# Kernel tuning notes

Measured on AMD Instinct MI355X. Metric: run time of the kernel, lower is better.

## Reference

```python
import jax, jax.numpy as jnp
import numpy as np

EPS = 1e-6
NUM_HEADS = 8
FOCUS = 3.0


def setup_inputs() -> dict:
    key = jax.random.key(0)
    ks = jax.random.split(key, 8)
    B, N, C = 16, 4096, 256
    head_dim, ksz = C // NUM_HEADS, 5
    s = 1.0 / np.sqrt(C)
    return {
        "x": jax.random.normal(ks[0], (B, N, C), jnp.float32),
        "Wq": jax.random.normal(ks[1], (C, C), jnp.float32) * s,
        "Wkv": jax.random.normal(ks[2], (C, 2 * C), jnp.float32) * s,
        "Wp": jax.random.normal(ks[3], (C, C), jnp.float32) * s,
        "bp": jnp.zeros((C,), jnp.float32),
        "scale_param": jnp.zeros((1, 1, C), jnp.float32),
        "pos_enc": jax.random.normal(ks[4], (1, N, C), jnp.float32) * 0.02,
        "dwc_w": jax.random.normal(ks[5], (head_dim, 1, ksz, ksz), jnp.float32) * 0.1,
        "dwc_b": jnp.zeros((head_dim,), jnp.float32),
        "H": 64,
        "W": 64,
    }


def _focus(t, scale, f):
    # relu feature map + power focusing with norm restoration
    t = (jax.nn.relu(t) + EPS) / scale
    tn = jnp.linalg.norm(t, axis=-1, keepdims=True)
    tf = t ** f
    return tf / jnp.linalg.norm(tf, axis=-1, keepdims=True) * tn


def reference(x, Wq, Wkv, Wp, bp, scale_param, pos_enc, dwc_w, dwc_b, H, W):
    B, N, C = x.shape
    h = NUM_HEADS
    d = C // h
    n = N  # sr_ratio == 1

    q = x @ Wq                                  # [B,N,C]
    kv = x @ Wkv                                # [B,N,2C]
    k, v = kv[..., :C], kv[..., C:]
    k = k + pos_enc

    scale = jax.nn.softplus(scale_param)
    q = _focus(q, scale, FOCUS)
    k = _focus(k, scale, FOCUS)

    # split heads: [B,h,N,d]
    qh = q.reshape(B, N, h, d).transpose(0, 2, 1, 3)
    kh = k.reshape(B, n, h, d).transpose(0, 2, 1, 3)
    vh = v.reshape(B, n, h, d).transpose(0, 2, 1, 3)

    # linear attention: z = 1/(q . mean_n(k)), kv = k^T v / n, out = (q @ kv) * z
    z = 1.0 / (jnp.einsum("bhnd,bhd->bhn", qh, kh.mean(axis=2)) + EPS)
    kvmat = jnp.einsum("bhnd,bhne->bhde", kh, vh) / n     # [B,h,d,d]
    out = jnp.einsum("bhnd,bhde->bhne", qh, kvmat) * z[..., None]

    out = out.transpose(0, 2, 1, 3).reshape(B, N, C)      # [B,N,C]

    # depthwise conv on v over the HxW grid, per head-channel
    v4 = vh.reshape(B * h, H, W, d).transpose(0, 3, 1, 2)  # [B*h,d,H,W]
    conv = jax.lax.conv_general_dilated(
        v4, dwc_w, window_strides=(1, 1), padding="SAME",
        feature_group_count=d,
        dimension_numbers=("NCHW", "OIHW", "NCHW"))
    conv = conv + dwc_b[None, :, None, None]
    out = out + conv.reshape(B, C, N).transpose(0, 2, 1)

    return out @ Wp + bp
```

## Files before the change

kernel.cpp:

```cpp
#include <hip/hip_runtime.h>
#include <hip/hip_bf16.h>

typedef unsigned short u16;
using bf16_t = __hip_bfloat16;
typedef short short8 __attribute__((ext_vector_type(8)));
typedef float f32x4 __attribute__((ext_vector_type(4)));

__device__ __forceinline__ float b2f(u16 u) {
    return __uint_as_float((unsigned int)u << 16);
}
__device__ __forceinline__ u16 f2b(float f) {
    bf16_t h = __float2bfloat16(f);
    union { bf16_t h; u16 u; } cv; cv.h = h; return cv.u;
}
__device__ __forceinline__ float ldv(const void* p, size_t i, int f32) {
    return f32 ? ((const float*)p)[i] : b2f(((const u16*)p)[i]);
}
__device__ __forceinline__ uint4 pack8(float4 a, float4 b) {
    uint4 u;
    u.x = (unsigned)f2b(a.x) | ((unsigned)f2b(a.y) << 16);
    u.y = (unsigned)f2b(a.z) | ((unsigned)f2b(a.w) << 16);
    u.z = (unsigned)f2b(b.x) | ((unsigned)f2b(b.y) << 16);
    u.w = (unsigned)f2b(b.z) | ((unsigned)f2b(b.w) << 16);
    return u;
}
__device__ __forceinline__ int swz(int n, int k) {
    return k ^ ((n & 7) << 3);
}
__device__ __forceinline__ void gl16(const u16* g, u16* l) {
    __builtin_amdgcn_global_load_lds(
        (const __attribute__((address_space(1))) unsigned int*)g,
        (__attribute__((address_space(3))) unsigned int*)l, 16, 0, 0);
}

__global__ void detect_kernel(const void* __restrict__ x, int* __restrict__ flag)
{
    const int t = threadIdx.x;
    const u16 h = ((const u16*)x)[2 * t];
    const int e = (h >> 7) & 0xFF;
    const int plaus = (e >= 112 && e <= 133) ? 1 : 0;
    const unsigned long long m = __ballot(plaus);
    if (t == 0) flag[0] = (__popcll(m) < 32) ? 1 : 0;
}

__global__ __launch_bounds__(256)
void xcvt_kernel(const void* __restrict__ x, u16* __restrict__ xb,
                 const int* __restrict__ flagp)
{
    const size_t i = ((size_t)blockIdx.x * 256 + threadIdx.x) * 8;
    if (*flagp) {
        const float* xf = (const float*)x + i;
        const float4 f0 = *reinterpret_cast<const float4*>(xf);
        const float4 f1 = *reinterpret_cast<const float4*>(xf + 4);
        *reinterpret_cast<uint4*>(xb + i) = pack8(f0, f1);
    } else {
        *reinterpret_cast<uint4*>(xb + i) =
            *reinterpret_cast<const uint4*>((const u16*)x + i);
    }
}

__global__ __launch_bounds__(256)
void prep_kernel(const void* __restrict__ pe, u16* __restrict__ peb,
                 const void* __restrict__ Wq, u16* __restrict__ WqT,
                 const void* __restrict__ Wkv, u16* __restrict__ WkvT,
                 const void* __restrict__ Wp, u16* __restrict__ WpT,
                 const int* __restrict__ flagp)
{
    const int f32 = *flagp;
    __shared__ float tile[32][33];
    const int bid = blockIdx.x;
    if (bid < 1024) {
        const size_t i = ((size_t)bid * 256 + threadIdx.x) * 4;
        if (f32) {
            const float4 f = *reinterpret_cast<const float4*>((const float*)pe + i);
            ushort4 o; o.x = f2b(f.x); o.y = f2b(f.y); o.z = f2b(f.z); o.w = f2b(f.w);
            *reinterpret_cast<ushort4*>(peb + i) = o;
        } else {
            *reinterpret_cast<ushort4*>(peb + i) =
                *reinterpret_cast<const ushort4*>((const u16*)pe + i);
        }
        return;
    }
    int lb = bid - 1024;
    const void* W; u16* WT; int N;
    if (lb < 64)       { W = Wq;  WT = WqT;  N = 256; }
    else if (lb < 192) { W = Wkv; WT = WkvT; N = 512; lb -= 64; }
    else               { W = Wp;  WT = WpT;  N = 256; lb -= 192; }
    const int tx = threadIdx.x & 31, ty = threadIdx.x >> 5;
    const int bx = lb % (N >> 5);
    const int by = lb / (N >> 5);
    #pragma unroll
    for (int r = 0; r < 4; ++r) {
        const int k = by * 32 + ty + r * 8;
        const int n = bx * 32 + tx;
        tile[ty + r * 8][tx] = ldv(W, (size_t)k * N + n, f32);
    }
    __syncthreads();
    #pragma unroll
    for (int r = 0; r < 4; ++r) {
        const int n2 = bx * 32 + ty + r * 8;
        const int k2 = by * 32 + tx;
        WT[(size_t)n2 * 256 + k2] = f2b(tile[tx][ty + r * 8]);
    }
}

template<int MODE>
__global__ __launch_bounds__(256, 2)
void gemm256(const void* __restrict__ Aany, const u16* __restrict__ Abf,
             const u16* __restrict__ BT, u16* __restrict__ O0,
             const void* __restrict__ extra, const int* __restrict__ flagp,
             int abf)
{
    const int f32 = *flagp;
    __shared__ u16 As[128 * 64];
    __shared__ u16 Bs[256 * 64];
    __shared__ float red2[2][128];
    __shared__ float red6[2][128];
    __shared__ float ratio_s[128];
    __shared__ float sscr[256];

    const int tid  = threadIdx.x;
    const int row0 = blockIdx.x * 128;
    const int lane = tid & 63;
    const int wv   = tid >> 6;
    const int wvu  = __builtin_amdgcn_readfirstlane(wv);
    const int wm   = (wv & 1) * 64;
    const int wn   = (wv >> 1) * 128;
    const int l15  = lane & 15;
    const int lq   = lane >> 4;
    const int lr8  = lane >> 3;
    const int lc8  = (lane & 7) * 8;

    if (MODE == 3) {
        const float p = ldv(extra, tid, f32);
        const float s = (p > 20.f) ? p : log1pf(expf(p));
        sscr[tid] = 1.0f / s;
    }

    f32x4 acc[4][8] = {};

    for (int k0 = 0; k0 < 256; k0 += 64) {
        #pragma unroll
        for (int it = 0; it < 8; ++it) {
            const int r = wvu * 64 + it * 8 + lr8;
            gl16(BT + (size_t)r * 256 + k0 + swz(r, lc8),
                 &Bs[(wvu * 64 + it * 8) * 64]);
        }
        if (MODE == 2 || abf || !f32) {
            const u16* Ab = (MODE == 2) ? Abf : (const u16*)Aany;
            #pragma unroll
            for (int it = 0; it < 4; ++it) {
                const int r = wvu * 32 + it * 8 + lr8;
                gl16(Ab + (size_t)(row0 + r) * 256 + k0 + swz(r, lc8),
                     &As[(wvu * 32 + it * 8) * 64]);
            }
        } else {
            const int sr = tid >> 1;
            const int sk = (tid & 1) * 32;
            const float* ag = (const float*)Aany +
                              (size_t)(row0 + sr) * 256 + k0 + sk;
            #pragma unroll
            for (int j = 0; j < 4; ++j) {
                const float4 f0 = *reinterpret_cast<const float4*>(ag + j * 8);
                const float4 f1 = *reinterpret_cast<const float4*>(ag + j * 8 + 4);
                *reinterpret_cast<uint4*>(
                    &As[sr * 64 + swz(sr, sk + j * 8)]) = pack8(f0, f1);
            }
        }
        __syncthreads();
        #pragma unroll
        for (int ks = 0; ks < 64; ks += 32) {
            const int ko = ks + lq * 8;
            short8 av[4], bv[8];
            #pragma unroll
            for (int i = 0; i < 4; ++i) {
                const int m = wm + i * 16 + l15;
                av[i] = *reinterpret_cast<const short8*>(&As[m * 64 + swz(m, ko)]);
            }
            #pragma unroll
            for (int j = 0; j < 8; ++j) {
                const int n = wn + j * 16 + l15;
                bv[j] = *reinterpret_cast<const short8*>(&Bs[n * 64 + swz(n, ko)]);
            }
            #pragma unroll
            for (int i = 0; i < 4; ++i)
                #pragma unroll
                for (int j = 0; j < 8; ++j)
                    acc[i][j] = __builtin_amdgcn_mfma_f32_16x16x32_bf16(
                        av[i], bv[j], acc[i][j], 0, 0, 0);
        }
        __syncthreads();
    }

    if (MODE == 3) {
        #pragma unroll
        for (int i = 0; i < 4; ++i) {
            #pragma unroll
            for (int rg = 0; rg < 4; ++rg) {
                const int lr = wm + i * 16 + lq * 4 + rg;
                float s2 = 0.f, s6 = 0.f;
                #pragma unroll
                for (int j = 0; j < 8; ++j) {
                    const int col = wn + j * 16 + l15;
                    const float xv =
                        (fmaxf(acc[i][j][rg], 0.f) + 1e-6f) * sscr[col];
                    acc[i][j][rg] = xv;
                    const float x2 = xv * xv;
                    s2 += x2;
                    s6 += x2 * x2 * x2;
                }
                #pragma unroll
                for (int off = 1; off < 16; off <<= 1) {
                    s2 += __shfl_xor(s2, off);
                    s6 += __shfl_xor(s6, off);
                }
                if (l15 == 0) { red2[wv >> 1][lr] = s2; red6[wv >> 1][lr] = s6; }
            }
        }
        __syncthreads();
        if (tid < 128)
            ratio_s[tid] = sqrtf((red2[0][tid] + red2[1][tid]) /
                                 (red6[0][tid] + red6[1][tid]));
        __syncthreads();
    }

    #pragma unroll
    for (int i = 0; i < 4; ++i) {
        #pragma unroll
        for (int j = 0; j < 8; ++j) {
            const int gcol = wn + j * 16 + l15;
            #pragma unroll
            for (int rg = 0; rg < 4; ++rg) {
                const int lr = wm + i * 16 + lq * 4 + rg;
                const size_t oi = (size_t)(row0 + lr) * 256 + gcol;
                const float a = acc[i][j][rg];
                if (MODE == 0) {
                    O0[oi] = f2b(a);
                } else if (MODE == 3) {
                    O0[oi] = f2b(a * a * a * ratio_s[lr]);
                } else {
                    const float o = a + ldv(extra, gcol, f32);
                    if (f32) ((float*)O0)[oi] = o;
                    else     O0[oi] = f2b(o);
                }
            }
        }
    }
}

__global__ __launch_bounds__(256, 2)
void fusedk_kernel(const void* __restrict__ x, const u16* __restrict__ WkvT,
                   const u16* __restrict__ peb, const u16* __restrict__ v,
                   const void* __restrict__ sp,
                   float* __restrict__ kvsm, float* __restrict__ ksm,
                   const int* __restrict__ flagp, int abf)
{
    const int f32 = *flagp;
    __shared__ u16 smem[24576];
    __shared__ float red2[4][64];
    __shared__ float red6[4][64];
    __shared__ float ratio_s[64];
    __shared__ float sscr[256];
    u16* As  = smem;
    u16* Bs  = smem + 8192;
    u16* KsT = smem;
    u16* VsT = smem + 16384;

    const int tid  = threadIdx.x;
    const int lane = tid & 63;
    const int wv   = tid >> 6;
    const int wvu  = __builtin_amdgcn_readfirstlane(wv);
    const int l15  = lane & 15;
    const int lq   = lane >> 4;
    const int wn   = wv * 64;
    const int lr8  = lane >> 3;
    const int lc8  = (lane & 7) * 8;

    {
        const float p = ldv(sp, tid, f32);
        const float s = (p > 20.f) ? p : log1pf(expf(p));
        sscr[tid] = 1.0f / s;
    }

    f32x4 cc[2][4] = {};
    float ksp[4] = {0.f, 0.f, 0.f, 0.f};

    const int b    = blockIdx.x >> 5;
    const int row0 = blockIdx.x * 128;

    f32x4 acc[2][4][4] = {};
    for (int k0 = 0; k0 < 256; k0 += 64) {
        #pragma unroll
        for (int it = 0; it < 8; ++it) {
            const int r = wvu * 64 + it * 8 + lr8;
            gl16(WkvT + (size_t)r * 256 + k0 + swz(r, lc8),
                 &Bs[(wvu * 64 + it * 8) * 64]);
        }
        if (abf || !f32) {
            #pragma unroll
            for (int it = 0; it < 4; ++it) {
                const int r = wvu * 32 + it * 8 + lr8;
                gl16((const u16*)x + (size_t)(row0 + r) * 256 + k0 + swz(r, lc8),
                     &As[(wvu * 32 + it * 8) * 64]);
            }
        } else {
            const int sr = tid >> 1;
            const int sk = (tid & 1) * 32;
            const float* ag = (const float*)x +
                              (size_t)(row0 + sr) * 256 + k0 + sk;
            #pragma unroll
            for (int j = 0; j < 4; ++j) {
                const float4 f0 = *reinterpret_cast<const float4*>(ag + j * 8);
                const float4 f1 = *reinterpret_cast<const float4*>(ag + j * 8 + 4);
                *reinterpret_cast<uint4*>(
                    &As[sr * 64 + swz(sr, sk + j * 8)]) = pack8(f0, f1);
            }
        }
        __syncthreads();
        #pragma unroll
        for (int c = 0; c < 2; ++c) {
            #pragma unroll
            for (int ks = 0; ks < 64; ks += 32) {
                const int ko = ks + lq * 8;
                short8 av[4], bvv[4];
                #pragma unroll
                for (int i = 0; i < 4; ++i) {
                    const int m = c * 64 + i * 16 + l15;
                    av[i] = *reinterpret_cast<const short8*>(&As[m * 64 + swz(m, ko)]);
                }
                #pragma unroll
                for (int j = 0; j < 4; ++j) {
                    const int n = wn + j * 16 + l15;
                    bvv[j] = *reinterpret_cast<const short8*>(&Bs[n * 64 + swz(n, ko)]);
                }
                #pragma unroll
                for (int i = 0; i < 4; ++i)
                    #pragma unroll
                    for (int j = 0; j < 4; ++j)
                        acc[c][i][j] = __builtin_amdgcn_mfma_f32_16x16x32_bf16(
                            av[i], bvv[j], acc[c][i][j], 0, 0, 0);
            }
        }
        __syncthreads();
    }

    #pragma unroll
    for (int c = 0; c < 2; ++c) {
        const int nb = (row0 & 4095) + c * 64;

        #pragma unroll
        for (int i = 0; i < 4; ++i) {
            #pragma unroll
            for (int rg = 0; rg < 4; ++rg) {
                const int lrow = i * 16 + lq * 4 + rg;
                float s2 = 0.f, s6 = 0.f;
                #pragma unroll
                for (int j = 0; j < 4; ++j) {
                    const int col = wn + j * 16 + l15;
                    const float t = acc[c][i][j][rg] +
                        b2f(peb[(size_t)(nb + lrow) * 256 + col]);
                    const float xv = (fmaxf(t, 0.f) + 1e-6f) * sscr[col];
                    acc[c][i][j][rg] = xv;
                    const float x2 = xv * xv;
                    s2 += x2;
                    s6 += x2 * x2 * x2;
                }
                #pragma unroll
                for (int off = 1; off < 16; off <<= 1) {
                    s2 += __shfl_xor(s2, off);
                    s6 += __shfl_xor(s6, off);
                }
                if (l15 == 0) { red2[wv][lrow] = s2; red6[wv][lrow] = s6; }
            }
        }
        __syncthreads();
        if (tid < 64) {
            const float s2t = red2[0][tid] + red2[1][tid] + red2[2][tid] + red2[3][tid];
            const float s6t = red6[0][tid] + red6[1][tid] + red6[2][tid] + red6[3][tid];
            ratio_s[tid] = sqrtf(s2t / s6t);
        }
        __syncthreads();

        {
            float kscol[4] = {0.f, 0.f, 0.f, 0.f};
            #pragma unroll
            for (int i = 0; i < 4; ++i)
                #pragma unroll
                for (int rg = 0; rg < 4; ++rg) {
                    const int lrow = i * 16 + lq * 4 + rg;
                    const float rt = ratio_s[lrow];
                    #pragma unroll
                    for (int j = 0; j < 4; ++j) {
                        const float xv = acc[c][i][j][rg];
                        const float kf = xv * xv * xv * rt;
                        const int d = wn + j * 16 + l15;
                        KsT[d * 64 + swz(d, lrow)] = f2b(kf);
                        kscol[j] += kf;
                    }
                }
            #pragma unroll
            for (int j = 0; j < 4; ++j) {
                float kp = kscol[j];
                kp += __shfl_xor(kp, 16);
                kp += __shfl_xor(kp, 32);
                ksp[j] += kp;
            }
        }

        #pragma unroll
        for (int p = 0; p < 2; ++p) {
            {
                const u16* vg = v + (size_t)(row0 + c * 64 + lane) * 256 +
                                p * 128 + wv * 32;
                uint4 t0[4];
                #pragma unroll
                for (int j = 0; j < 4; ++j)
                    t0[j] = *reinterpret_cast<const uint4*>(vg + j * 8);
                #pragma unroll
                for (int j = 0; j < 4; ++j) {
                    const u16* pp = (const u16*)&t0[j];
                    #pragma unroll
                    for (int m = 0; m < 8; ++m) {
                        const int el = wv * 32 + j * 8 + m;
                        VsT[el * 64 + swz(el, lane)] = pp[m];
                    }
                }
            }
            __syncthreads();
            {
                const int h  = p * 4 + wv;
                const int cb = h * 32;
                const int el = wv * 32;
                #pragma unroll
                for (int kk = 0; kk < 64; kk += 32) {
                    const int ko = kk + lq * 8;
                    const short8 a0 = *reinterpret_cast<const short8*>(
                        &KsT[(cb + l15) * 64 + swz(cb + l15, ko)]);
                    const short8 a1 = *reinterpret_cast<const short8*>(
                        &KsT[(cb + 16 + l15) * 64 + swz(cb + 16 + l15, ko)]);
                    const short8 b0 = *reinterpret_cast<const short8*>(
                        &VsT[(el + l15) * 64 + swz(el + l15, ko)]);
                    const short8 b1 = *reinterpret_cast<const short8*>(
                        &VsT[(el + 16 + l15) * 64 + swz(el + 16 + l15, ko)]);
                    cc[p][0] = __builtin_amdgcn_mfma_f32_16x16x32_bf16(a0, b0, cc[p][0], 0, 0, 0);
                    cc[p][1] = __builtin_amdgcn_mfma_f32_16x16x32_bf16(a0, b1, cc[p][1], 0, 0, 0);
                    cc[p][2] = __builtin_amdgcn_mfma_f32_16x16x32_bf16(a1, b0, cc[p][2], 0, 0, 0);
                    cc[p][3] = __builtin_amdgcn_mfma_f32_16x16x32_bf16(a1, b1, cc[p][3], 0, 0, 0);
                }
            }
            __syncthreads();
        }
    }

    const int slot = blockIdx.x & 1;
    float* ksb = ksm + (size_t)(slot * 16 + b) * 256;
    #pragma unroll
    for (int j = 0; j < 4; ++j)
        if (lane < 16)
            atomicAdd(&ksb[wn + j * 16 + lane], ksp[j]);
    #pragma unroll
    for (int hh = 0; hh < 2; ++hh) {
        const int h = hh * 4 + wv;
        float* base = kvsm + ((size_t)(slot * 16 + b) * 8 + h) * 1024;
        #pragma unroll
        for (int rg = 0; rg < 4; ++rg) {
            const int d0 = lq * 4 + rg;
            atomicAdd(&base[(size_t)d0 * 32 + l15],             cc[hh][0][rg]);
            atomicAdd(&base[(size_t)d0 * 32 + 16 + l15],        cc[hh][1][rg]);
            atomicAdd(&base[(size_t)(d0 + 16) * 32 + l15],      cc[hh][2][rg]);
            atomicAdd(&base[(size_t)(d0 + 16) * 32 + 16 + l15], cc[hh][3][rg]);
        }
    }
}

__global__ __launch_bounds__(256, 2)
void attn_mfma_kernel(u16* __restrict__ qy, const float* __restrict__ kvsum,
                      const float* __restrict__ ksum)
{
    __shared__ u16 qs[64 * 256];
    __shared__ u16 kvT[8 * 32 * 40];
    __shared__ float km[8][32];
    __shared__ float zds[64][8];
    const int tid  = threadIdx.x;
    const int lane = tid & 63;
    const int wv   = tid >> 6;
    const int wvu  = __builtin_amdgcn_readfirstlane(wv);
    const int l15  = lane & 15;
    const int lq   = lane >> 4;
    const int b    = blockIdx.x >> 6;
    const int n0   = (blockIdx.x & 63) * 64;
    const float inv_n = 1.0f / 4096.0f;

    {
        const int qr2 = lane >> 5;
        const int qc8 = (lane & 31) * 8;
        const u16* qb = qy + (size_t)(b * 4096 + n0) * 256;
        #pragma unroll
        for (int it = 0; it < 8; ++it) {
            const int r = wvu * 16 + it * 2 + qr2;
            gl16(qb + (size_t)r * 256 + (qc8 ^ ((r & 7) << 3)),
                 &qs[(wvu * 16 + it * 2) * 256]);
        }
    }
    {
        const int h = tid >> 5, e = tid & 31;
        const float* k0 = kvsum + (size_t)b * 8192 + h * 1024 + e;
        const float* k1 = kvsum + (size_t)(16 + b) * 8192 + h * 1024 + e;
        #pragma unroll
        for (int d = 0; d < 32; ++d)
            kvT[h * 1280 + e * 40 + d] = f2b((k0[d * 32] + k1[d * 32]) * inv_n);
        (&km[0][0])[tid] = (ksum[(size_t)b * 256 + tid] +
                            ksum[(size_t)(16 + b) * 256 + tid]) * inv_n;
    }
    __syncthreads();

    {
        const int zt = tid & 63;
        const int zh0 = (tid >> 6) * 2;
        #pragma unroll
        for (int hh = 0; hh < 2; ++hh) {
            const int h = zh0 + hh;
            float s = 0.f;
            #pragma unroll
            for (int d = 0; d < 32; ++d) {
                const int col = (h * 32 + d) ^ ((zt & 7) << 3);
                s = fmaf(b2f(qs[zt * 256 + col]), km[h][d], s);
            }
            zds[zt][h] = s;
        }
    }

    f32x4 acc[8][2];
    #pragma unroll
    for (int h = 0; h < 8; ++h) {
        const int m = wvu * 16 + l15;
        const int col = (h * 32 + lq * 8) ^ ((m & 7) << 3);
        const short8 av = *reinterpret_cast<const short8*>(&qs[m * 256 + col]);
        const short8 b0 = *reinterpret_cast<const short8*>(
            &kvT[h * 1280 + l15 * 40 + lq * 8]);
        const short8 b1 = *reinterpret_cast<const short8*>(
            &kvT[h * 1280 + (16 + l15) * 40 + lq * 8]);
        const f32x4 z = {0.f, 0.f, 0.f, 0.f};
        acc[h][0] = __builtin_amdgcn_mfma_f32_16x16x32_bf16(av, b0, z, 0, 0, 0);
        acc[h][1] = __builtin_amdgcn_mfma_f32_16x16x32_bf16(av, b1, z, 0, 0, 0);
    }
    __syncthreads();

    u16* qb = qy + (size_t)(b * 4096 + n0) * 256;
    #pragma unroll
    for (int h = 0; h < 8; ++h) {
        #pragma unroll
        for (int eh = 0; eh < 2; ++eh) {
            const int gcol = h * 32 + eh * 16 + l15;
            #pragma unroll
            for (int rg = 0; rg < 4; ++rg) {
                const int lr = wvu * 16 + lq * 4 + rg;
                const float z = 1.0f / (zds[lr][h] + 1e-6f);
                qb[(size_t)lr * 256 + gcol] = f2b(acc[h][eh][rg] * z);
            }
        }
    }
}

__global__ __launch_bounds__(256, 2)
void conv_add_kernel(const u16* __restrict__ v, const void* __restrict__ w,
                     const void* __restrict__ bias, u16* __restrict__ y,
                     const int* __restrict__ flagp)
{
    const int f32 = *flagp;
    __shared__ u16 vt[144 * 256];
    __shared__ float wl[800];
    __shared__ float bl[32];
    const int tid = threadIdx.x;
    for (int i = tid; i < 800; i += 256) wl[i] = ldv(w, i, f32);
    if (tid < 32) bl[tid] = ldv(bias, tid, f32);

    const int bb = blockIdx.x >> 6;
    const int ty = (blockIdx.x >> 3) & 7;
    const int tx = blockIdx.x & 7;
    const int y0 = ty * 8, x0 = tx * 8;
    const u16* vb = v + (size_t)bb * 4096 * 256;

    #pragma unroll
    for (int it = 0; it < 18; ++it) {
        const int idx = it * 256 + tid;
        const int px  = idx >> 5;
        const int c8  = (idx & 31) * 8;
        const int py  = px / 12, pxx = px - py * 12;
        const int yy = y0 + py - 2, xx = x0 + pxx - 2;
        uint4 val = {0u, 0u, 0u, 0u};
        if (yy >= 0 && yy < 64 && xx >= 0 && xx < 64)
            val = *reinterpret_cast<const uint4*>(
                vb + (size_t)((yy << 6) + xx) * 256 + c8);
        *reinterpret_cast<uint4*>(&vt[px * 256 + c8]) = val;
    }
    __syncthreads();

    const int c  = tid;
    const int dc = c & 31;
    float wreg[25];
    #pragma unroll
    for (int i = 0; i < 25; ++i) wreg[i] = wl[dc * 25 + i];
    const float bv = bl[dc];

    float win[5][12];
    #pragma unroll
    for (int r = 0; r < 5; ++r)
        #pragma unroll
        for (int cc = 0; cc < 12; ++cc)
            win[r][cc] = b2f(vt[(r * 12 + cc) * 256 + c]);

    u16* yb = y + ((size_t)bb * 4096 + (size_t)y0 * 64 + x0) * 256 + c;
    #pragma unroll
    for (int oy = 0; oy < 8; ++oy) {
        if (oy) {
            #pragma unroll
            for (int r = 0; r < 4; ++r)
                #pragma unroll
                for (int cc = 0; cc < 12; ++cc) win[r][cc] = win[r + 1][cc];
            #pragma unroll
            for (int cc = 0; cc < 12; ++cc)
                win[4][cc] = b2f(vt[((oy + 4) * 12 + cc) * 256 + c]);
        }
        #pragma unroll
        for (int ox = 0; ox < 8; ++ox) {
            float s = 0.f;
            #pragma unroll
            for (int ky = 0; ky < 5; ++ky)
                #pragma unroll
                for (int kx = 0; kx < 5; ++kx)
                    s = fmaf(win[oy ? ky : ky][ox + kx], wreg[ky * 5 + kx], s);
            u16* yp = yb + (size_t)(oy * 64 + ox) * 256;
            *yp = f2b(b2f(*yp) + s + bv);
        }
    }
}

extern "C" void kernel_launch(void* const* d_in, const int* in_sizes, int n_in,
                              void* d_out, int out_size, void* d_ws, size_t ws_size,
                              hipStream_t stream)
{
    (void)in_sizes; (void)n_in; (void)out_size;
    const void* x   = d_in[0];
    const void* Wq  = d_in[1];
    const void* Wkv = d_in[2];
    const void* Wp  = d_in[3];
    const void* bp  = d_in[4];
    const void* sp  = d_in[5];
    const void* pe  = d_in[6];
    const void* dw  = d_in[7];
    const void* db  = d_in[8];

    int*   flag = (int*)d_ws;
    float* kvsm = (float*)((char*)d_ws + 64);
    float* ksm  = kvsm + 262144;
    u16*   WqT  = (u16*)(ksm + 8192);
    u16*   WkvT = WqT + 65536;
    u16*   WpT  = WkvT + 131072;
    u16*   peb  = WpT + 65536;
    u16*   qy   = peb + 1048576;
    u16*   xb   = qy + (size_t)16777216;
    u16*   v    = (u16*)d_out;

    const size_t need = (size_t)((char*)(xb + 16777216) - (char*)d_ws);
    const int big = (ws_size >= need) ? 1 : 0;

    hipMemsetAsync(kvsm, 0, (262144 + 8192) * sizeof(float), stream);
    detect_kernel<<<1, 64, 0, stream>>>(x, flag);
    if (big) xcvt_kernel<<<8192, 256, 0, stream>>>(x, xb, flag);
    prep_kernel<<<1280, 256, 0, stream>>>(pe, peb, Wq, WqT, Wkv, WkvT,
                                          Wp, WpT, flag);

    const void* Ax = big ? (const void*)xb : x;

    hipLaunchKernelGGL((gemm256<3>), dim3(512), dim3(256), 0, stream,
                       Ax, (const u16*)nullptr, WqT, qy, sp, flag, big);
    hipLaunchKernelGGL((gemm256<0>), dim3(512), dim3(256), 0, stream,
                       Ax, (const u16*)nullptr, WkvT + (size_t)256 * 256, v,
                       (const void*)nullptr, flag, big);
    fusedk_kernel<<<512, 256, 0, stream>>>(Ax, WkvT, peb, v, sp, kvsm, ksm,
                                           flag, big);

    attn_mfma_kernel<<<1024, 256, 0, stream>>>(qy, kvsm, ksm);
    conv_add_kernel<<<1024, 256, 0, stream>>>(v, dw, db, qy, flag);
    hipLaunchKernelGGL((gemm256<2>), dim3(512), dim3(256), 0, stream,
                       (const void*)nullptr, qy, WpT, (u16*)d_out, bp, flag, 0);
}
```

Baseline: 312.2 us.

## Halve GEMM row tile to 64 and double grid size across projection kernels

Shrinks the row tile in the projection GEMMs and the fused K/KV kernel from 128 to 64 rows, doubling the number of blocks from 512 to 1024 so the GPU's compute units are filled more evenly. Each wave now covers all 64 rows and a 64-column slice, with the row-norm reduction spread across four waves. The KV partial-sum buffers grow to four slots per batch, and the attention kernel sums four partials instead of two. The cost is that B-matrix tiles (the weights) are reloaded twice as often per output row, lowering reuse per block.

Measured after the change: 324.2 us. 3.8% more time.

```diff
diff --git a/kernel.cpp b/kernel.cpp
--- a/kernel.cpp
+++ b/kernel.cpp
@@ -112,20 +112,19 @@
              int abf)
 {
     const int f32 = *flagp;
-    __shared__ u16 As[128 * 64];
+    __shared__ u16 As[64 * 64];
     __shared__ u16 Bs[256 * 64];
-    __shared__ float red2[2][128];
-    __shared__ float red6[2][128];
-    __shared__ float ratio_s[128];
+    __shared__ float red2[4][64];
+    __shared__ float red6[4][64];
+    __shared__ float ratio_s[64];
     __shared__ float sscr[256];
 
     const int tid  = threadIdx.x;
-    const int row0 = blockIdx.x * 128;
+    const int row0 = blockIdx.x * 64;
     const int lane = tid & 63;
     const int wv   = tid >> 6;
     const int wvu  = __builtin_amdgcn_readfirstlane(wv);
-    const int wm   = (wv & 1) * 64;
-    const int wn   = (wv >> 1) * 128;
+    const int wn   = wv * 64;
     const int l15  = lane & 15;
     const int lq   = lane >> 4;
     const int lr8  = lane >> 3;
@@ -137,7 +136,7 @@
         sscr[tid] = 1.0f / s;
     }
 
-    f32x4 acc[4][8] = {};
+    f32x4 acc[4][4] = {};
 
     for (int k0 = 0; k0 < 256; k0 += 64) {
         #pragma unroll
@@ -149,43 +148,42 @@
         if (MODE == 2 || abf || !f32) {
             const u16* Ab = (MODE == 2) ? Abf : (const u16*)Aany;
             #pragma unroll
-            for (int it = 0; it < 4; ++it) {
-                const int r = wvu * 32 + it * 8 + lr8;
+            for (int it = 0; it < 2; ++it) {
+                const int r = wvu * 16 + it * 8 + lr8;
                 gl16(Ab + (size_t)(row0 + r) * 256 + k0 + swz(r, lc8),
-                     &As[(wvu * 32 + it * 8) * 64]);
+                     &As[(wvu * 16 + it * 8) * 64]);
             }
         } else {
-            const int sr = tid >> 1;
-            const int sk = (tid & 1) * 32;
+            const int ar = tid >> 2, ak = (tid & 3) * 16;
             const float* ag = (const float*)Aany +
-                              (size_t)(row0 + sr) * 256 + k0 + sk;
-            #pragma unroll
-            for (int j = 0; j < 4; ++j) {
+                              (size_t)(row0 + ar) * 256 + k0 + ak;
+            #pragma unroll
+            for (int j = 0; j < 2; ++j) {
                 const float4 f0 = *reinterpret_cast<const float4*>(ag + j * 8);
                 const float4 f1 = *reinterpret_cast<const float4*>(ag + j * 8 + 4);
                 *reinterpret_cast<uint4*>(
-                    &As[sr * 64 + swz(sr, sk + j * 8)]) = pack8(f0, f1);
+                    &As[ar * 64 + swz(ar, ak + j * 8)]) = pack8(f0, f1);
             }
         }
         __syncthreads();
         #pragma unroll
         for (int ks = 0; ks < 64; ks += 32) {
             const int ko = ks + lq * 8;
-            short8 av[4], bv[8];
+            short8 av[4], bv[4];
             #pragma unroll
             for (int i = 0; i < 4; ++i) {
-                const int m = wm + i * 16 + l15;
+                const int m = i * 16 + l15;
                 av[i] = *reinterpret_cast<const short8*>(&As[m * 64 + swz(m, ko)]);
             }
             #pragma unroll
-            for (int j = 0; j < 8; ++j) {
+            for (int j = 0; j < 4; ++j) {
                 const int n = wn + j * 16 + l15;
                 bv[j] = *reinterpret_cast<const short8*>(&Bs[n * 64 + swz(n, ko)]);
             }
             #pragma unroll
             for (int i = 0; i < 4; ++i)
                 #pragma unroll
-                for (int j = 0; j < 8; ++j)
+                for (int j = 0; j < 4; ++j)
                     acc[i][j] = __builtin_amdgcn_mfma_f32_16x16x32_bf16(
                         av[i], bv[j], acc[i][j], 0, 0, 0);
         }
@@ -197,10 +195,10 @@
         for (int i = 0; i < 4; ++i) {
             #pragma unroll
             for (int rg = 0; rg < 4; ++rg) {
-                const int lr = wm + i * 16 + lq * 4 + rg;
+                const int lr = i * 16 + lq * 4 + rg;
                 float s2 = 0.f, s6 = 0.f;
                 #pragma unroll
-                for (int j = 0; j < 8; ++j) {
+                for (int j = 0; j < 4; ++j) {
                     const int col = wn + j * 16 + l15;
                     const float xv =
                         (fmaxf(acc[i][j][rg], 0.f) + 1e-6f) * sscr[col];
@@ -214,24 +212,26 @@
                     s2 += __shfl_xor(s2, off);
                     s6 += __shfl_xor(s6, off);
                 }
-                if (l15 == 0) { red2[wv >> 1][lr] = s2; red6[wv >> 1][lr] = s6; }
-            }
-        }
-        __syncthreads();
-        if (tid < 128)
-            ratio_s[tid] = sqrtf((red2[0][tid] + red2[1][tid]) /
-                                 (red6[0][tid] + red6[1][tid]));
+                if (l15 == 0) { red2[wv][lr] = s2; red6[wv][lr] = s6; }
+            }
+        }
+        __syncthreads();
+        if (tid < 64) {
+            const float s2t = red2[0][tid] + red2[1][tid] + red2[2][tid] + red2[3][tid];
+            const float s6t = red6[0][tid] + red6[1][tid] + red6[2][tid] + red6[3][tid];
+            ratio_s[tid] = sqrtf(s2t / s6t);
+        }
         __syncthreads();
     }
 
     #pragma unroll
     for (int i = 0; i < 4; ++i) {
         #pragma unroll
-        for (int j = 0; j < 8; ++j) {
+        for (int j = 0; j < 4; ++j) {
             const int gcol = wn + j * 16 + l15;
             #pragma unroll
             for (int rg = 0; rg < 4; ++rg) {
-                const int lr = wm + i * 16 + lq * 4 + rg;
+                const int lr = i * 16 + lq * 4 + rg;
                 const size_t oi = (size_t)(row0 + lr) * 256 + gcol;
                 const float a = acc[i][j][rg];
                 if (MODE == 0) {
@@ -262,7 +262,7 @@
     __shared__ float ratio_s[64];
     __shared__ float sscr[256];
     u16* As  = smem;
-    u16* Bs  = smem + 8192;
+    u16* Bs  = smem + 4096;
     u16* KsT = smem;
     u16* VsT = smem + 16384;
 
@@ -285,10 +285,11 @@
     f32x4 cc[2][4] = {};
     float ksp[4] = {0.f, 0.f, 0.f, 0.f};
 
-    const int b    = blockIdx.x >> 5;
-    const int row0 = blockIdx.x * 128;
-
-    f32x4 acc[2][4][4] = {};
+    const int b    = blockIdx.x >> 6;
+    const int row0 = blockIdx.x * 64;
+    const int nb   = row0 & 4095;
+
+    f32x4 acc[4][4] = {};
     for (int k0 = 0; k0 < 256; k0 += 64) {
         #pragma unroll
         for (int it = 0; it < 8; ++it) {
@@ -298,161 +299,151 @@
         }
         if (abf || !f32) {
             #pragma unroll
-            for (int it = 0; it < 4; ++it) {
-                const int r = wvu * 32 + it * 8 + lr8;
+            for (int it = 0; it < 2; ++it) {
+                const int r = wvu * 16 + it * 8 + lr8;
                 gl16((const u16*)x + (size_t)(row0 + r) * 256 + k0 + swz(r, lc8),
-                     &As[(wvu * 32 + it * 8) * 64]);
+                     &As[(wvu * 16 + it * 8) * 64]);
             }
         } else {
-            const int sr = tid >> 1;
-            const int sk = (tid & 1) * 32;
+            const int ar = tid >> 2, ak = (tid & 3) * 16;
             const float* ag = (const float*)x +
-                              (size_t)(row0 + sr) * 256 + k0 + sk;
-            #pragma unroll
-            for (int j = 0; j < 4; ++j) {
+                              (size_t)(row0 + ar) * 256 + k0 + ak;
+            #pragma unroll
+            for (int j = 0; j < 2; ++j) {
                 const float4 f0 = *reinterpret_cast<const float4*>(ag + j * 8);
                 const float4 f1 = *reinterpret_cast<const float4*>(ag + j * 8 + 4);
                 *reinterpret_cast<uint4*>(
-                    &As[sr * 64 + swz(sr, sk + j * 8)]) = pack8(f0, f1);
-            }
-        }
-        __syncthreads();
-        #pragma unroll
-        for (int c = 0; c < 2; ++c) {
-            #pragma unroll
-            for (int ks = 0; ks < 64; ks += 32) {
-                const int ko = ks + lq * 8;
-                short8 av[4], bvv[4];
-                #pragma unroll
-                for (int i = 0; i < 4; ++i) {
-                    const int m = c * 64 + i * 16 + l15;
-                    av[i] = *reinterpret_cast<const short8*>(&As[m * 64 + swz(m, ko)]);
-                }
-                #pragma unroll
-                for (int j = 0; j < 4; ++j) {
-                    const int n = wn + j * 16 + l15;
-                    bvv[j] = *reinterpret_cast<const short8*>(&Bs[n * 64 + swz(n, ko)]);
-                }
-                #pragma unroll
-                for (int i = 0; i < 4; ++i)
-                    #pragma unroll
-                    for (int j = 0; j < 4; ++j)
-                        acc[c][i][j] = __builtin_amdgcn_mfma_f32_16x16x32_bf16(
-                            av[i], bvv[j], acc[c][i][j], 0, 0, 0);
-            }
-        }
-        __syncthreads();
-    }
-
-    #pragma unroll
-    for (int c = 0; c < 2; ++c) {
-        const int nb = (row0 & 4095) + c * 64;
-
-        #pragma unroll
-        for (int i = 0; i < 4; ++i) {
+                    &As[ar * 64 + swz(ar, ak + j * 8)]) = pack8(f0, f1);
+            }
+        }
+        __syncthreads();
+        #pragma unroll
+        for (int ks = 0; ks < 64; ks += 32) {
+            const int ko = ks + lq * 8;
+            short8 av[4], bvv[4];
+            #pragma unroll
+            for (int i = 0; i < 4; ++i) {
+                const int m = i * 16 + l15;
+                av[i] = *reinterpret_cast<const short8*>(&As[m * 64 + swz(m, ko)]);
+            }
+            #pragma unroll
+            for (int j = 0; j < 4; ++j) {
+                const int n = wn + j * 16 + l15;
+                bvv[j] = *reinterpret_cast<const short8*>(&Bs[n * 64 + swz(n, ko)]);
+            }
+            #pragma unroll
+            for (int i = 0; i < 4; ++i)
+                #pragma unroll
+                for (int j = 0; j < 4; ++j)
+                    acc[i][j] = __builtin_amdgcn_mfma_f32_16x16x32_bf16(
+                        av[i], bvv[j], acc[i][j], 0, 0, 0);
+        }
+        __syncthreads();
+    }
+
+    #pragma unroll
+    for (int i = 0; i < 4; ++i) {
+        #pragma unroll
+        for (int rg = 0; rg < 4; ++rg) {
+            const int lrow = i * 16 + lq * 4 + rg;
+            float s2 = 0.f, s6 = 0.f;
+            #pragma unroll
+            for (int j = 0; j < 4; ++j) {
+                const int col = wn + j * 16 + l15;
+                const float t = acc[i][j][rg] +
+                    b2f(peb[(size_t)(nb + lrow) * 256 + col]);
+                const float xv = (fmaxf(t, 0.f) + 1e-6f) * sscr[col];
+                acc[i][j][rg] = xv;
+                const float x2 = xv * xv;
+                s2 += x2;
+                s6 += x2 * x2 * x2;
+            }
+            #pragma unroll
+            for (int off = 1; off < 16; off <<= 1) {
+                s2 += __shfl_xor(s2, off);
+                s6 += __shfl_xor(s6, off);
+            }
+            if (l15 == 0) { red2[wv][lrow] = s2; red6[wv][lrow] = s6; }
+        }
+    }
+    __syncthreads();
+    if (tid < 64) {
+        const float s2t = red2[0][tid] + red2[1][tid] + red2[2][tid] + red2[3][tid];
+        const float s6t = red6[0][tid] + red6[1][tid] + red6[2][tid] + red6[3][tid];
+        ratio_s[tid] = sqrtf(s2t / s6t);
+    }
+    __syncthreads();
+
+    {
+        float kscol[4] = {0.f, 0.f, 0.f, 0.f};
+        #pragma unroll
+        for (int i = 0; i < 4; ++i)
             #pragma unroll
             for (int rg = 0; rg < 4; ++rg) {
                 const int lrow = i * 16 + lq * 4 + rg;
-                float s2 = 0.f, s6 = 0.f;
+                const float rt = ratio_s[lrow];
                 #pragma unroll
                 for (int j = 0; j < 4; ++j) {
-                    const int col = wn + j * 16 + l15;
-                    const float t = acc[c][i][j][rg] +
-                        b2f(peb[(size_t)(nb + lrow) * 256 + col]);
-                    const float xv = (fmaxf(t, 0.f) + 1e-6f) * sscr[col];
-                    acc[c][i][j][rg] = xv;
-                    const float x2 = xv * xv;
-                    s2 += x2;
-                    s6 += x2 * x2 * x2;
+                    const float xv = acc[i][j][rg];
+                    const float kf = xv * xv * xv * rt;
+                    const int d = wn + j * 16 + l15;
+                    KsT[d * 64 + swz(d, lrow)] = f2b(kf);
+                    kscol[j] += kf;
                 }
-                #pragma unroll
-                for (int off = 1; off < 16; off <<= 1) {
-                    s2 += __shfl_xor(s2, off);
-                    s6 += __shfl_xor(s6, off);
+            }
+        #pragma unroll
+        for (int j = 0; j < 4; ++j) {
+            float kp = kscol[j];
+            kp += __shfl_xor(kp, 16);
+            kp += __shfl_xor(kp, 32);
+            ksp[j] = kp;
+        }
+    }
+
+    #pragma unroll
+    for (int p = 0; p < 2; ++p) {
+        {
+            const u16* vg = v + (size_t)(row0 + lane) * 256 + p * 128 + wv * 32;
+            uint4 t0[4];
+            #pragma unroll
+            for (int j = 0; j < 4; ++j)
+                t0[j] = *reinterpret_cast<const uint4*>(vg + j * 8);
+            #pragma unroll
+            for (int j = 0; j < 4; ++j) {
+                const u16* pp = (const u16*)&t0[j];
+                #pragma unroll
+                for (int m = 0; m < 8; ++m) {
+                    const int el = wv * 32 + j * 8 + m;
+                    VsT[el * 64 + swz(el, lane)] = pp[m];
                 }
-                if (l15 == 0) { red2[wv][lrow] = s2; red6[wv][lrow] = s6; }
-            }
-        }
-        __syncthreads();
-        if (tid < 64) {
-            const float s2t = red2[0][tid] + red2[1][tid] + red2[2][tid] + red2[3][tid];
-            const float s6t = red6[0][tid] + red6[1][tid] + red6[2][tid] + red6[3][tid];
-            ratio_s[tid] = sqrtf(s2t / s6t);
-        }
-        __syncthreads();
-
+            }
+        }
+        __syncthreads();
         {
-            float kscol[4] = {0.f, 0.f, 0.f, 0.f};
-            #pragma unroll
-            for (int i = 0; i < 4; ++i)
-                #pragma unroll
-                for (int rg = 0; rg < 4; ++rg) {
-                    const int lrow = i * 16 + lq * 4 + rg;
-                    const float rt = ratio_s[lrow];
-                    #pragma unroll
-                    for (int j = 0; j < 4; ++j) {
-                        const float xv = acc[c][i][j][rg];
-                        const float kf = xv * xv * xv * rt;
-                        const int d = wn + j * 16 + l15;
-                        KsT[d * 64 + swz(d, lrow)] = f2b(kf);
-                        kscol[j] += kf;
-                    }
-                }
-            #pragma unroll
-            for (int j = 0; j < 4; ++j) {
-                float kp = kscol[j];
-                kp += __shfl_xor(kp, 16);
-                kp += __shfl_xor(kp, 32);
-                ksp[j] += kp;
-            }
-        }
-
-        #pragma unroll
-        for (int p = 0; p < 2; ++p) {
-            {
-                const u16* vg = v + (size_t)(row0 + c * 64 + lane) * 256 +
-                                p * 128 + wv * 32;
-                uint4 t0[4];
-                #pragma unroll
-                for (int j = 0; j < 4; ++j)
-                    t0[j] = *reinterpret_cast<const uint4*>(vg + j * 8);
-                #pragma unroll
-                for (int j = 0; j < 4; ++j) {
-                    const u16* pp = (const u16*)&t0[j];
-                    #pragma unroll
-                    for (int m = 0; m < 8; ++m) {
-                        const int el = wv * 32 + j * 8 + m;
-                        VsT[el * 64 + swz(el, lane)] = pp[m];
-                    }
-                }
-            }
-            __syncthreads();
-            {
-                const int h  = p * 4 + wv;
-                const int cb = h * 32;
-                const int el = wv * 32;
-                #pragma unroll
-                for (int kk = 0; kk < 64; kk += 32) {
-                    const int ko = kk + lq * 8;
-                    const short8 a0 = *reinterpret_cast<const short8*>(
-                        &KsT[(cb + l15) * 64 + swz(cb + l15, ko)]);
-                    const short8 a1 = *reinterpret_cast<const short8*>(
-                        &KsT[(cb + 16 + l15) * 64 + swz(cb + 16 + l15, ko)]);
-                    const short8 b0 = *reinterpret_cast<const short8*>(
-                        &VsT[(el + l15) * 64 + swz(el + l15, ko)]);
-                    const short8 b1 = *reinterpret_cast<const short8*>(
-                        &VsT[(el + 16 + l15) * 64 + swz(el + 16 + l15, ko)]);
-                    cc[p][0] = __builtin_amdgcn_mfma_f32_16x16x32_bf16(a0, b0, cc[p][0], 0, 0, 0);
-                    cc[p][1] = __builtin_amdgcn_mfma_f32_16x16x32_bf16(a0, b1, cc[p][1], 0, 0, 0);
-                    cc[p][2] = __builtin_amdgcn_mfma_f32_16x16x32_bf16(a1, b0, cc[p][2], 0, 0, 0);
-                    cc[p][3] = __builtin_amdgcn_mfma_f32_16x16x32_bf16(a1, b1, cc[p][3], 0, 0, 0);
-                }
-            }
-            __syncthreads();
-        }
-    }
-
-    const int slot = blockIdx.x & 1;
+            const int h  = p * 4 + wv;
+            const int cb = h * 32;
+            const int el = wv * 32;
+            #pragma unroll
+            for (int kk = 0; kk < 64; kk += 32) {
+                const int ko = kk + lq * 8;
+                const short8 a0 = *reinterpret_cast<const short8*>(
+                    &KsT[(cb + l15) * 64 + swz(cb + l15, ko)]);
+                const short8 a1 = *reinterpret_cast<const short8*>(
+                    &KsT[(cb + 16 + l15) * 64 + swz(cb + 16 + l15, ko)]);
+                const short8 b0 = *reinterpret_cast<const short8*>(
+                    &VsT[(el + l15) * 64 + swz(el + l15, ko)]);
+                const short8 b1 = *reinterpret_cast<const short8*>(
+                    &VsT[(el + 16 + l15) * 64 + swz(el + 16 + l15, ko)]);
+                cc[p][0] = __builtin_amdgcn_mfma_f32_16x16x32_bf16(a0, b0, cc[p][0], 0, 0, 0);
+                cc[p][1] = __builtin_amdgcn_mfma_f32_16x16x32_bf16(a0, b1, cc[p][1], 0, 0, 0);
+                cc[p][2] = __builtin_amdgcn_mfma_f32_16x16x32_bf16(a1, b0, cc[p][2], 0, 0, 0);
+                cc[p][3] = __builtin_amdgcn_mfma_f32_16x16x32_bf16(a1, b1, cc[p][3], 0, 0, 0);
+            }
+        }
+        __syncthreads();
+    }
+
+    const int slot = blockIdx.x & 3;
     float* ksb = ksm + (size_t)(slot * 16 + b) * 256;
     #pragma unroll
     for (int j = 0; j < 4; ++j)
@@ -504,13 +495,19 @@
     }
     {
         const int h = tid >> 5, e = tid & 31;
-        const float* k0 = kvsum + (size_t)b * 8192 + h * 1024 + e;
-        const float* k1 = kvsum + (size_t)(16 + b) * 8192 + h * 1024 + e;
-        #pragma unroll
-        for (int d = 0; d < 32; ++d)
-            kvT[h * 1280 + e * 40 + d] = f2b((k0[d * 32] + k1[d * 32]) * inv_n);
+        const float* kp = kvsum + (size_t)b * 8192 + h * 1024 + e;
+        #pragma unroll
+        for (int d = 0; d < 32; ++d) {
+            const float s = kp[d * 32] +
+                            kp[(size_t)16 * 8192 + d * 32] +
+                            kp[(size_t)32 * 8192 + d * 32] +
+                            kp[(size_t)48 * 8192 + d * 32];
+            kvT[h * 1280 + e * 40 + d] = f2b(s * inv_n);
+        }
         (&km[0][0])[tid] = (ksum[(size_t)b * 256 + tid] +
-                            ksum[(size_t)(16 + b) * 256 + tid]) * inv_n;
+                            ksum[(size_t)(16 + b) * 256 + tid] +
+                            ksum[(size_t)(32 + b) * 256 + tid] +
+                            ksum[(size_t)(48 + b) * 256 + tid]) * inv_n;
     }
     __syncthreads();
 
@@ -629,7 +626,7 @@
             for (int ky = 0; ky < 5; ++ky)
                 #pragma unroll
                 for (int kx = 0; kx < 5; ++kx)
-                    s = fmaf(win[oy ? ky : ky][ox + kx], wreg[ky * 5 + kx], s);
+                    s = fmaf(win[ky][ox + kx], wreg[ky * 5 + kx], s);
             u16* yp = yb + (size_t)(oy * 64 + ox) * 256;
             *yp = f2b(b2f(*yp) + s + bv);
         }
@@ -653,8 +650,8 @@
 
     int*   flag = (int*)d_ws;
     float* kvsm = (float*)((char*)d_ws + 64);
-    float* ksm  = kvsm + 262144;
-    u16*   WqT  = (u16*)(ksm + 8192);
+    float* ksm  = kvsm + 524288;
+    u16*   WqT  = (u16*)(ksm + 16384);
     u16*   WkvT = WqT + 65536;
     u16*   WpT  = WkvT + 131072;
     u16*   peb  = WpT + 65536;
@@ -665,7 +662,7 @@
     const size_t need = (size_t)((char*)(xb + 16777216) - (char*)d_ws);
     const int big = (ws_size >= need) ? 1 : 0;
 
-    hipMemsetAsync(kvsm, 0, (262144 + 8192) * sizeof(float), stream);
+    hipMemsetAsync(kvsm, 0, (524288 + 16384) * sizeof(float), stream);
     detect_kernel<<<1, 64, 0, stream>>>(x, flag);
     if (big) xcvt_kernel<<<8192, 256, 0, stream>>>(x, xb, flag);
     prep_kernel<<<1280, 256, 0, stream>>>(pe, peb, Wq, WqT, Wkv, WkvT,
@@ -673,16 +670,16 @@
 
     const void* Ax = big ? (const void*)xb : x;
 
-    hipLaunchKernelGGL((gemm256<3>), dim3(512), dim3(256), 0, stream,
+    hipLaunchKernelGGL((gemm256<3>), dim3(1024), dim3(256), 0, stream,
                        Ax, (const u16*)nullptr, WqT, qy, sp, flag, big);
-    hipLaunchKernelGGL((gemm256<0>), dim3(512), dim3(256), 0, stream,
+    hipLaunchKernelGGL((gemm256<0>), dim3(1024), dim3(256), 0, stream,
                        Ax, (const u16*)nullptr, WkvT + (size_t)256 * 256, v,
                        (const void*)nullptr, flag, big);
-    fusedk_kernel<<<512, 256, 0, stream>>>(Ax, WkvT, peb, v, sp, kvsm, ksm,
-                                           flag, big);
+    fusedk_kernel<<<1024, 256, 0, stream>>>(Ax, WkvT, peb, v, sp, kvsm, ksm,
+                                            flag, big);
 
     attn_mfma_kernel<<<1024, 256, 0, stream>>>(qy, kvsm, ksm);
     conv_add_kernel<<<1024, 256, 0, stream>>>(v, dw, db, qy, flag);
-    hipLaunchKernelGGL((gemm256<2>), dim3(512), dim3(256), 0, stream,
+    hipLaunchKernelGGL((gemm256<2>), dim3(1024), dim3(256), 0, stream,
                        (const void*)nullptr, qy, WpT, (u16*)d_out, bp, flag, 0);
 }
```

## Double-buffer LDS K-tiles in GEMM kernels to overlap loads with MFMA

Applied to the files above, without the earlier changes.

Both the gemm256 and fusedk kernels now split K into 32-wide tiles staged into two alternating LDS buffers. The loads for the next tile are issued before the MFMAs on the current one, so the block syncs once per tile instead of twice, and global-to-LDS transfer can overlap compute. The swizzle changes to match the 32-column rows. Iteration count doubles with smaller tiles, and the fp32 A path still stalls on synchronous loads.

New measurement: 308.5 us. Within noise of the previous version (-1.2%).

```diff
diff --git a/kernel.cpp b/kernel.cpp
--- a/kernel.cpp
+++ b/kernel.cpp
@@ -26,6 +26,9 @@
 }
 __device__ __forceinline__ int swz(int n, int k) {
     return k ^ ((n & 7) << 3);
+}
+__device__ __forceinline__ int swz32(int n, int kblk) {
+    return (kblk ^ (n & 3)) << 3;
 }
 __device__ __forceinline__ void gl16(const u16* g, u16* l) {
     __builtin_amdgcn_global_load_lds(
@@ -112,8 +115,7 @@
              int abf)
 {
     const int f32 = *flagp;
-    __shared__ u16 As[128 * 64];
-    __shared__ u16 Bs[256 * 64];
+    __shared__ u16 smem[24576];
     __shared__ float red2[2][128];
     __shared__ float red6[2][128];
     __shared__ float ratio_s[128];
@@ -128,8 +130,8 @@
     const int wn   = (wv >> 1) * 128;
     const int l15  = lane & 15;
     const int lq   = lane >> 4;
-    const int lr8  = lane >> 3;
-    const int lc8  = (lane & 7) * 8;
+    const int lr4  = lane >> 2;
+    const int lb3  = lane & 3;
 
     if (MODE == 3) {
         const float p = ldv(extra, tid, f32);
@@ -137,58 +139,64 @@
         sscr[tid] = 1.0f / s;
     }
 
-    f32x4 acc[4][8] = {};
-
-    for (int k0 = 0; k0 < 256; k0 += 64) {
-        #pragma unroll
-        for (int it = 0; it < 8; ++it) {
-            const int r = wvu * 64 + it * 8 + lr8;
-            gl16(BT + (size_t)r * 256 + k0 + swz(r, lc8),
-                 &Bs[(wvu * 64 + it * 8) * 64]);
-        }
-        if (MODE == 2 || abf || !f32) {
-            const u16* Ab = (MODE == 2) ? Abf : (const u16*)Aany;
-            #pragma unroll
-            for (int it = 0; it < 4; ++it) {
-                const int r = wvu * 32 + it * 8 + lr8;
-                gl16(Ab + (size_t)(row0 + r) * 256 + k0 + swz(r, lc8),
-                     &As[(wvu * 32 + it * 8) * 64]);
+    const int use_dma_a = (MODE == 2) || abf || !f32;
+    const u16* Ab = (MODE == 2) ? Abf : (const u16*)Aany;
+
+    auto stage = [&](int k0, int buf) {
+        u16* As = smem + buf * 12288;
+        u16* Bs = As + 4096;
+        #pragma unroll
+        for (int d = 0; d < 4; ++d) {
+            const int r = wvu * 64 + d * 16 + lr4;
+            gl16(BT + (size_t)r * 256 + k0 + swz32(r, lb3),
+                 &Bs[(wvu * 64 + d * 16) * 32]);
+        }
+        if (use_dma_a) {
+            #pragma unroll
+            for (int d = 0; d < 2; ++d) {
+                const int r = wvu * 32 + d * 16 + lr4;
+                gl16(Ab + (size_t)(row0 + r) * 256 + k0 + swz32(r, lb3),
+                     &As[(wvu * 32 + d * 16) * 32]);
             }
         } else {
-            const int sr = tid >> 1;
-            const int sk = (tid & 1) * 32;
+            const int sr = tid >> 1, skb = (tid & 1) * 2;
             const float* ag = (const float*)Aany +
-                              (size_t)(row0 + sr) * 256 + k0 + sk;
-            #pragma unroll
-            for (int j = 0; j < 4; ++j) {
+                              (size_t)(row0 + sr) * 256 + k0 + skb * 8;
+            #pragma unroll
+            for (int j = 0; j < 2; ++j) {
                 const float4 f0 = *reinterpret_cast<const float4*>(ag + j * 8);
                 const float4 f1 = *reinterpret_cast<const float4*>(ag + j * 8 + 4);
                 *reinterpret_cast<uint4*>(
-                    &As[sr * 64 + swz(sr, sk + j * 8)]) = pack8(f0, f1);
-            }
-        }
-        __syncthreads();
-        #pragma unroll
-        for (int ks = 0; ks < 64; ks += 32) {
-            const int ko = ks + lq * 8;
-            short8 av[4], bv[8];
-            #pragma unroll
-            for (int i = 0; i < 4; ++i) {
-                const int m = wm + i * 16 + l15;
-                av[i] = *reinterpret_cast<const short8*>(&As[m * 64 + swz(m, ko)]);
-            }
-            #pragma unroll
-            for (int j = 0; j < 8; ++j) {
-                const int n = wn + j * 16 + l15;
-                bv[j] = *reinterpret_cast<const short8*>(&Bs[n * 64 + swz(n, ko)]);
-            }
-            #pragma unroll
-            for (int i = 0; i < 4; ++i)
-                #pragma unroll
-                for (int j = 0; j < 8; ++j)
-                    acc[i][j] = __builtin_amdgcn_mfma_f32_16x16x32_bf16(
-                        av[i], bv[j], acc[i][j], 0, 0, 0);
-        }
+                    &As[sr * 32 + swz32(sr, skb + j)]) = pack8(f0, f1);
+            }
+        }
+    };
+
+    f32x4 acc[4][8] = {};
+
+    stage(0, 0);
+    __syncthreads();
+    for (int t = 0; t < 8; ++t) {
+        if (t < 7) stage((t + 1) * 32, (t + 1) & 1);
+        const u16* As = smem + (t & 1) * 12288;
+        const u16* Bs = As + 4096;
+        short8 av[4], bv[8];
+        #pragma unroll
+        for (int i = 0; i < 4; ++i) {
+            const int m = wm + i * 16 + l15;
+            av[i] = *reinterpret_cast<const short8*>(&As[m * 32 + swz32(m, lq)]);
+        }
+        #pragma unroll
+        for (int j = 0; j < 8; ++j) {
+            const int n = wn + j * 16 + l15;
+            bv[j] = *reinterpret_cast<const short8*>(&Bs[n * 32 + swz32(n, lq)]);
+        }
+        #pragma unroll
+        for (int i = 0; i < 4; ++i)
+            #pragma unroll
+            for (int j = 0; j < 8; ++j)
+                acc[i][j] = __builtin_amdgcn_mfma_f32_16x16x32_bf16(
+                    av[i], bv[j], acc[i][j], 0, 0, 0);
         __syncthreads();
     }
 
@@ -261,8 +269,6 @@
     __shared__ float red6[4][64];
     __shared__ float ratio_s[64];
     __shared__ float sscr[256];
-    u16* As  = smem;
-    u16* Bs  = smem + 8192;
     u16* KsT = smem;
     u16* VsT = smem + 16384;
 
@@ -273,8 +279,8 @@
     const int l15  = lane & 15;
     const int lq   = lane >> 4;
     const int wn   = wv * 64;
-    const int lr8  = lane >> 3;
-    const int lc8  = (lane & 7) * 8;
+    const int lr4  = lane >> 2;
+    const int lb3  = lane & 3;
 
     {
         const float p = ldv(sp, tid, f32);
@@ -288,58 +294,63 @@
     const int b    = blockIdx.x >> 5;
     const int row0 = blockIdx.x * 128;
 
-    f32x4 acc[2][4][4] = {};
-    for (int k0 = 0; k0 < 256; k0 += 64) {
-        #pragma unroll
-        for (int it = 0; it < 8; ++it) {
-            const int r = wvu * 64 + it * 8 + lr8;
-            gl16(WkvT + (size_t)r * 256 + k0 + swz(r, lc8),
-                 &Bs[(wvu * 64 + it * 8) * 64]);
+    auto stage = [&](int k0, int buf) {
+        u16* As = smem + buf * 12288;
+        u16* Bs = As + 4096;
+        #pragma unroll
+        for (int d = 0; d < 4; ++d) {
+            const int r = wvu * 64 + d * 16 + lr4;
+            gl16(WkvT + (size_t)r * 256 + k0 + swz32(r, lb3),
+                 &Bs[(wvu * 64 + d * 16) * 32]);
         }
         if (abf || !f32) {
             #pragma unroll
-            for (int it = 0; it < 4; ++it) {
-                const int r = wvu * 32 + it * 8 + lr8;
-                gl16((const u16*)x + (size_t)(row0 + r) * 256 + k0 + swz(r, lc8),
-                     &As[(wvu * 32 + it * 8) * 64]);
+            for (int d = 0; d < 2; ++d) {
+                const int r = wvu * 32 + d * 16 + lr4;
+                gl16((const u16*)x + (size_t)(row0 + r) * 256 + k0 + swz32(r, lb3),
+                     &As[(wvu * 32 + d * 16) * 32]);
             }
         } else {
-            const int sr = tid >> 1;
-            const int sk = (tid & 1) * 32;
+            const int sr = tid >> 1, skb = (tid & 1) * 2;
             const float* ag = (const float*)x +
-                              (size_t)(row0 + sr) * 256 + k0 + sk;
-            #pragma unroll
-            for (int j = 0; j < 4; ++j) {
+                              (size_t)(row0 + sr) * 256 + k0 + skb * 8;
+            #pragma unroll
+            for (int j = 0; j < 2; ++j) {
                 const float4 f0 = *reinterpret_cast<const float4*>(ag + j * 8);
                 const float4 f1 = *reinterpret_cast<const float4*>(ag + j * 8 + 4);
                 *reinterpret_cast<uint4*>(
-                    &As[sr * 64 + swz(sr, sk + j * 8)]) = pack8(f0, f1);
-            }
-        }
-        __syncthreads();
+                    &As[sr * 32 + swz32(sr, skb + j)]) = pack8(f0, f1);
+            }
+        }
+    };
+
+    f32x4 acc[2][4][4] = {};
+    stage(0, 0);
+    __syncthreads();
+    for (int t = 0; t < 8; ++t) {
+        if (t < 7) stage((t + 1) * 32, (t + 1) & 1);
+        const u16* As = smem + (t & 1) * 12288;
+        const u16* Bs = As + 4096;
+        short8 bvv[4];
+        #pragma unroll
+        for (int j = 0; j < 4; ++j) {
+            const int n = wn + j * 16 + l15;
+            bvv[j] = *reinterpret_cast<const short8*>(&Bs[n * 32 + swz32(n, lq)]);
+        }
         #pragma unroll
         for (int c = 0; c < 2; ++c) {
-            #pragma unroll
-            for (int ks = 0; ks < 64; ks += 32) {
-                const int ko = ks + lq * 8;
-                short8 av[4], bvv[4];
-                #pragma unroll
-                for (int i = 0; i < 4; ++i) {
-                    const int m = c * 64 + i * 16 + l15;
-                    av[i] = *reinterpret_cast<const short8*>(&As[m * 64 + swz(m, ko)]);
-                }
-                #pragma unroll
-                for (int j = 0; j < 4; ++j) {
-                    const int n = wn + j * 16 + l15;
-                    bvv[j] = *reinterpret_cast<const short8*>(&Bs[n * 64 + swz(n, ko)]);
-                }
-                #pragma unroll
-                for (int i = 0; i < 4; ++i)
-                    #pragma unroll
-                    for (int j = 0; j < 4; ++j)
-                        acc[c][i][j] = __builtin_amdgcn_mfma_f32_16x16x32_bf16(
-                            av[i], bvv[j], acc[c][i][j], 0, 0, 0);
-            }
+            short8 av[4];
+            #pragma unroll
+            for (int i = 0; i < 4; ++i) {
+                const int m = c * 64 + i * 16 + l15;
+                av[i] = *reinterpret_cast<const short8*>(&As[m * 32 + swz32(m, lq)]);
+            }
+            #pragma unroll
+            for (int i = 0; i < 4; ++i)
+                #pragma unroll
+                for (int j = 0; j < 4; ++j)
+                    acc[c][i][j] = __builtin_amdgcn_mfma_f32_16x16x32_bf16(
+                        av[i], bvv[j], acc[c][i][j], 0, 0, 0);
         }
         __syncthreads();
     }
@@ -629,7 +640,7 @@
             for (int ky = 0; ky < 5; ++ky)
                 #pragma unroll
                 for (int kx = 0; kx < 5; ++kx)
-                    s = fmaf(win[oy ? ky : ky][ox + kx], wreg[ky * 5 + kx], s);
+                    s = fmaf(win[ky][ox + kx], wreg[ky * 5 + kx], s);
             u16* yp = yb + (size_t)(oy * 64 + ox) * 256;
             *yp = f2b(b2f(*yp) + s + bv);
         }
```
